# Kernel tuning notes

Measured on AMD Instinct MI355X. Metric: run time of the kernel, lower is better.

Reference implementation:

```python
import jax, jax.numpy as jnp
import numpy as np

S, D_IN, D_OUT = 4096, 1024, 1024

def setup_inputs() -> dict:
    key = jax.random.key(0)
    kx, kq, kk, kv = jax.random.split(key, 4)
    scale = 0.02
    return {
        "x": jax.random.normal(kx, (S, D_IN), dtype=jnp.float32),
        "W_query": jax.random.normal(kq, (D_IN, D_OUT), dtype=jnp.float32) * scale,
        "W_key": jax.random.normal(kk, (D_IN, D_OUT), dtype=jnp.float32) * scale,
        "W_value": jax.random.normal(kv, (D_IN, D_OUT), dtype=jnp.float32) * scale,
    }

def reference(x, W_query, W_key, W_value):
    # x: [S, d_in]; W_*: [d_in, d_out]
    queries = x @ W_query        # [S, d_out]
    keys = x @ W_key             # [S, d_out]
    values = x @ W_value         # [S, d_out]
    d_k = keys.shape[-1]
    attn_scores = queries @ keys.T            # [S, S]
    attn_weights = jax.nn.softmax(attn_scores / jnp.sqrt(jnp.float32(d_k)), axis=-1)
    context_vec = attn_weights @ values       # [S, d_out]
    return context_vec
```

## Files before the change

kernel.cpp:

```cpp
#include <hip/hip_runtime.h>
#include <hip/hip_bf16.h>

typedef _Float16 f16x8 __attribute__((ext_vector_type(8)));
typedef float f32x4 __attribute__((ext_vector_type(4)));
typedef unsigned short u16;
typedef u16 u16x8 __attribute__((ext_vector_type(8)));
typedef u16 u16x4 __attribute__((ext_vector_type(4)));

__device__ __forceinline__ u16 f2h_bits(float f) {
    _Float16 h = (_Float16)f;
    return __builtin_bit_cast(u16, h);
}
__device__ __forceinline__ float h2f(u16 b) {
    return (float)__builtin_bit_cast(_Float16, b);
}

template <int MODE>
__global__ __launch_bounds__(256, 4) void gemm_bt(
    const u16* __restrict__ A, int lda,
    const u16* __restrict__ B, int ldb,
    u16* __restrict__ C, int ldc,
    int Ksplit, float alpha, size_t c_z_stride,
    int bnW, int bmW, int numPanelX,
    float* __restrict__ rowsum, u16* __restrict__ vt)
{
    __shared__ __attribute__((aligned(16))) u16 As[128 * 32];
    __shared__ __attribute__((aligned(16))) u16 Bs[128 * 32];

    const int t    = threadIdx.x;
    const int lane = t & 63;
    const int wave = t >> 6;
    const int wm   = wave & 1;
    const int wn   = wave >> 1;
    const int l16  = lane & 15;
    const int quad = lane >> 4;

    const int lin = blockIdx.y * gridDim.x + blockIdx.x;
    const int xcd = lin & 7;
    const int idx = lin >> 3;
    const int px  = xcd % numPanelX;
    const int py  = xcd / numPanelX;
    const int bn  = px * bnW + idx % bnW;
    const int bm  = py * bmW + idx / bnW;

    const int kz = blockIdx.z;
    A += (size_t)kz * Ksplit;
    B += (size_t)kz * Ksplit;
    C += (size_t)kz * c_z_stride;

    const int srow = t >> 2;
    const int scol = ((t & 3) ^ ((t >> 3) & 3)) * 8;

    const u16* Ag = A + (size_t)(bm * 128 + srow) * lda + scol;
    const u16* Bg = B + (size_t)(bn * 128 + srow) * ldb + scol;
    const size_t a64 = (size_t)64 * lda;
    const size_t b64 = (size_t)64 * ldb;

    u16* AsD = &As[t * 8];
    u16* BsD = &Bs[t * 8];

    const int fseg = (quad ^ ((l16 >> 1) & 3)) * 8;
    const u16* Afr = &As[(wm * 64 + l16) * 32 + fseg];
    const u16* Bfr = &Bs[(wn * 64 + l16) * 32 + fseg];

    f32x4 acc[4][4] = {};

    float4 a0A, a1A, b0A, b1A;
    float4 a0B, a1B, b0B, b1B;

    a0A = *(const float4*)(Ag);
    a1A = *(const float4*)(Ag + a64);
    b0A = *(const float4*)(Bg);
    b1A = *(const float4*)(Bg + b64);
    a0B = *(const float4*)(Ag + 32);
    a1B = *(const float4*)(Ag + 32 + a64);
    b0B = *(const float4*)(Bg + 32);
    b1B = *(const float4*)(Bg + 32 + b64);

    for (int k0 = 0; k0 < Ksplit; k0 += 64) {
        __syncthreads();
        *(float4*)(AsD)        = a0A;
        *(float4*)(AsD + 2048) = a1A;
        *(float4*)(BsD)        = b0A;
        *(float4*)(BsD + 2048) = b1A;
        __syncthreads();

        {
            const int kn = (k0 + 64 < Ksplit) ? k0 + 64 : 0;
            a0A = *(const float4*)(Ag + kn);
            a1A = *(const float4*)(Ag + kn + a64);
            b0A = *(const float4*)(Bg + kn);
            b1A = *(const float4*)(Bg + kn + b64);
        }

        {
            f16x8 af[4], bfv[4];
#pragma unroll
            for (int i = 0; i < 4; i++) af[i]  = *(const f16x8*)(Afr + i * 512);
#pragma unroll
            for (int i = 0; i < 4; i++) bfv[i] = *(const f16x8*)(Bfr + i * 512);
#pragma unroll
            for (int mi = 0; mi < 4; mi++)
#pragma unroll
                for (int ni = 0; ni < 4; ni++)
                    acc[mi][ni] = __builtin_amdgcn_mfma_f32_16x16x32_f16(
                        af[mi], bfv[ni], acc[mi][ni], 0, 0, 0);
        }

        __syncthreads();
        *(float4*)(AsD)        = a0B;
        *(float4*)(AsD + 2048) = a1B;
        *(float4*)(BsD)        = b0B;
        *(float4*)(BsD + 2048) = b1B;
        __syncthreads();

        {
            const int kn = (k0 + 96 < Ksplit) ? k0 + 96 : 0;
            a0B = *(const float4*)(Ag + kn);
            a1B = *(const float4*)(Ag + kn + a64);
            b0B = *(const float4*)(Bg + kn);
            b1B = *(const float4*)(Bg + kn + b64);
        }

        {
            f16x8 af[4], bfv[4];
#pragma unroll
            for (int i = 0; i < 4; i++) af[i]  = *(const f16x8*)(Afr + i * 512);
#pragma unroll
            for (int i = 0; i < 4; i++) bfv[i] = *(const f16x8*)(Bfr + i * 512);
#pragma unroll
            for (int mi = 0; mi < 4; mi++)
#pragma unroll
                for (int ni = 0; ni < 4; ni++)
                    acc[mi][ni] = __builtin_amdgcn_mfma_f32_16x16x32_f16(
                        af[mi], bfv[ni], acc[mi][ni], 0, 0, 0);
        }
    }

    const int crow = bm * 128 + wm * 64 + quad * 4;
    const int ccol = bn * 128 + wn * 64 + l16;

    if (MODE == 1) {
        float rs[4][4];
#pragma unroll
        for (int mi = 0; mi < 4; mi++)
#pragma unroll
            for (int r = 0; r < 4; r++) rs[mi][r] = 0.f;
#pragma unroll
        for (int mi = 0; mi < 4; mi++) {
#pragma unroll
            for (int ni = 0; ni < 4; ni++) {
#pragma unroll
                for (int r = 0; r < 4; r++) {
                    float e = __expf(acc[mi][ni][r] * alpha);
                    rs[mi][r] += e;
                    C[(size_t)(crow + mi * 16 + r) * ldc + (ccol + ni * 16)] = f2h_bits(e);
                }
            }
        }
#pragma unroll
        for (int mi = 0; mi < 4; mi++) {
#pragma unroll
            for (int r = 0; r < 4; r++) {
                float s = rs[mi][r];
#pragma unroll
                for (int o = 1; o < 16; o <<= 1) s += __shfl_xor(s, o);
                if (l16 == 0)
                    atomicAdd(&rowsum[crow + mi * 16 + r], s);
            }
        }
    } else if (MODE == 2 && bn >= 16) {
#pragma unroll
        for (int ni = 0; ni < 4; ni++) {
            const int cV = (bn - 16) * 128 + wn * 64 + ni * 16 + l16;
#pragma unroll
            for (int mi = 0; mi < 4; mi++) {
                u16x4 o;
#pragma unroll
                for (int r = 0; r < 4; r++) o[r] = f2h_bits(acc[mi][ni][r]);
                *(u16x4*)(vt + (size_t)cV * 4096 + crow + mi * 16) = o;
            }
        }
    } else {
#pragma unroll
        for (int mi = 0; mi < 4; mi++)
#pragma unroll
            for (int ni = 0; ni < 4; ni++)
#pragma unroll
                for (int r = 0; r < 4; r++)
                    C[(size_t)(crow + mi * 16 + r) * ldc + (ccol + ni * 16)] =
                        f2h_bits(acc[mi][ni][r] * alpha);
    }
}

__global__ __launch_bounds__(256) void cast_to_f16(
    const float* __restrict__ in, u16* __restrict__ out, int n)
{
    int i = (blockIdx.x * 256 + threadIdx.x) * 4;
    if (i + 3 < n) {
        float4 v = *(const float4*)(in + i);
        ushort4 o;
        o.x = f2h_bits(v.x);
        o.y = f2h_bits(v.y);
        o.z = f2h_bits(v.z);
        o.w = f2h_bits(v.w);
        *(ushort4*)(out + i) = o;
    }
}

__global__ __launch_bounds__(256) void transpose_w3(
    const float* __restrict__ W0, const float* __restrict__ W1,
    const float* __restrict__ W2, u16* __restrict__ out)
{
    const float* in = (blockIdx.z == 0) ? W0 : (blockIdx.z == 1) ? W1 : W2;
    u16* o = out + (size_t)blockIdx.z * 1024 * 1024;
    __shared__ float tile[32][33];
    const int bx = blockIdx.x * 32;
    const int by = blockIdx.y * 32;
    const int tx = threadIdx.x, ty = threadIdx.y;
#pragma unroll
    for (int j = 0; j < 4; j++)
        tile[ty + j * 8][tx] = in[(size_t)(by + ty + j * 8) * 1024 + bx + tx];
    __syncthreads();
#pragma unroll
    for (int j = 0; j < 4; j++)
        o[(size_t)(bx + ty + j * 8) * 1024 + by + tx] = f2h_bits(tile[tx][ty + j * 8]);
}

__global__ __launch_bounds__(256) void zero_f32(float* __restrict__ p, int n)
{
    int i = (blockIdx.x * 256 + threadIdx.x) * 4;
    if (i + 3 < n) *(float4*)(p + i) = float4{0.f, 0.f, 0.f, 0.f};
}

__global__ __launch_bounds__(256) void add_div4(
    const u16* __restrict__ P, const float* __restrict__ l,
    float* __restrict__ o)
{
    const size_t zs = (size_t)4096 * 1024;
    int i = (blockIdx.x * 256 + threadIdx.x) * 8;
    float inv = 1.0f / l[i >> 10];
    float s[8] = {};
#pragma unroll
    for (int z = 0; z < 4; z++) {
        u16x8 h = *(const u16x8*)(P + z * zs + i);
#pragma unroll
        for (int j = 0; j < 8; j++) s[j] += h2f(h[j]);
    }
    float4 lo{s[0] * inv, s[1] * inv, s[2] * inv, s[3] * inv};
    float4 hi{s[4] * inv, s[5] * inv, s[6] * inv, s[7] * inv};
    *(float4*)(o + i) = lo;
    *(float4*)(o + i + 4) = hi;
}

extern "C" void kernel_launch(void* const* d_in, const int* in_sizes, int n_in,
                              void* d_out, int out_size, void* d_ws, size_t ws_size,
                              hipStream_t stream)
{
    (void)in_sizes; (void)n_in; (void)out_size; (void)ws_size;
    const float* x  = (const float*)d_in[0];
    const float* Wq = (const float*)d_in[1];
    const float* Wk = (const float*)d_in[2];
    const float* Wv = (const float*)d_in[3];
    float* out = (float*)d_out;
    char* ws = (char*)d_ws;

    u16* xb  = (u16*)(ws);
    u16* Wt  = (u16*)(ws + ((size_t)8  << 20));
    u16* QK  = (u16*)(ws + ((size_t)14 << 20));
    u16* Sb  = (u16*)(ws + ((size_t)32 << 20));
    u16* Vt  = (u16*)(ws + ((size_t)64 << 20));
    float* lr = (float*)(ws + ((size_t)72 << 20));
    u16* P   = (u16*)(ws);

    const int S = 4096, D = 1024;
    dim3 tb(32, 8);

    cast_to_f16<<<(S * D) / (4 * 256), 256, 0, stream>>>(x, xb, S * D);

    transpose_w3<<<dim3(32, 32, 3), tb, 0, stream>>>(Wq, Wk, Wv, Wt);

    gemm_bt<2><<<dim3(3072 / 128, S / 128, 1), 256, 0, stream>>>(
        xb, D, Wt, D, QK, 2048, D, 1.0f, 0, 6, 16, 4, nullptr, Vt);

    zero_f32<<<S / (4 * 256), 256, 0, stream>>>(lr, S);

    gemm_bt<1><<<dim3(S / 128, S / 128, 1), 256, 0, stream>>>(
        QK, 2048, QK + 1024, 2048, Sb, S, D, 0.03125f, 0, 8, 16, 4, lr, nullptr);

    gemm_bt<0><<<dim3(D / 128, S / 128, 4), 256, 0, stream>>>(
        Sb, S, Vt, S, P, D, 1024, 1.0f, (size_t)S * D, 4, 8, 2, nullptr, nullptr);

    add_div4<<<(S * D) / (8 * 256), 256, 0, stream>>>(P, lr, out);
}
```

Before: 223.9 us.

## Rewrite GEMM as 256x256 tiles with direct global-to-LDS async double buffering

Replaces the 128x128, 4-wave GEMM with a 256x256, 8-wave tile that loads global memory straight into LDS via global_load_lds, double-buffered two k-tiles ahead with explicit vmcnt waits. The MFMA loop is split into four quadrant phases separated by barriers and setprio so LDS fragment reads and prefetches interleave with matrix ops. The aim is to cut register staging, raise arithmetic intensity per tile and hide memory latency. In exchange it uses 128KB of LDS per block, holds a larger accumulator, and launches fewer blocks (e.g. 192 for the QKV GEMM), which may underfill the GPU.

```diff
diff --git a/kernel.cpp b/kernel.cpp
--- a/kernel.cpp
+++ b/kernel.cpp
@@ -1,5 +1,4 @@
 #include <hip/hip_runtime.h>
-#include <hip/hip_bf16.h>
 
 typedef _Float16 f16x8 __attribute__((ext_vector_type(8)));
 typedef float f32x4 __attribute__((ext_vector_type(4)));
@@ -15,8 +14,14 @@
     return (float)__builtin_bit_cast(_Float16, b);
 }
 
+typedef __attribute__((address_space(1))) unsigned int gu32_as1;
+typedef __attribute__((address_space(3))) unsigned int lu32_as3;
+__device__ __forceinline__ void gload16(const u16* g, u16* l) {
+    __builtin_amdgcn_global_load_lds((gu32_as1*)g, (lu32_as3*)l, 16, 0, 0);
+}
+
 template <int MODE>
-__global__ __launch_bounds__(256, 4) void gemm_bt(
+__global__ __launch_bounds__(512, 2) void gemm_bt(
     const u16* __restrict__ A, int lda,
     const u16* __restrict__ B, int ldb,
     u16* __restrict__ C, int ldc,
@@ -24,14 +29,14 @@
     int bnW, int bmW, int numPanelX,
     float* __restrict__ rowsum, u16* __restrict__ vt)
 {
-    __shared__ __attribute__((aligned(16))) u16 As[128 * 32];
-    __shared__ __attribute__((aligned(16))) u16 Bs[128 * 32];
+    __shared__ __attribute__((aligned(16))) u16 As[32768];
+    __shared__ __attribute__((aligned(16))) u16 Bs[32768];
 
     const int t    = threadIdx.x;
     const int lane = t & 63;
     const int wave = t >> 6;
-    const int wm   = wave & 1;
-    const int wn   = wave >> 1;
+    const int wm   = wave >> 2;
+    const int wn   = wave & 3;
     const int l16  = lane & 15;
     const int quad = lane >> 4;
 
@@ -49,105 +54,151 @@
     C += (size_t)kz * c_z_stride;
 
     const int srow = t >> 2;
-    const int scol = ((t & 3) ^ ((t >> 3) & 3)) * 8;
-
-    const u16* Ag = A + (size_t)(bm * 128 + srow) * lda + scol;
-    const u16* Bg = B + (size_t)(bn * 128 + srow) * ldb + scol;
-    const size_t a64 = (size_t)64 * lda;
-    const size_t b64 = (size_t)64 * ldb;
-
-    u16* AsD = &As[t * 8];
-    u16* BsD = &Bs[t * 8];
-
-    const int fseg = (quad ^ ((l16 >> 1) & 3)) * 8;
-    const u16* Afr = &As[(wm * 64 + l16) * 32 + fseg];
-    const u16* Bfr = &Bs[(wn * 64 + l16) * 32 + fseg];
-
-    f32x4 acc[4][4] = {};
-
-    float4 a0A, a1A, b0A, b1A;
-    float4 a0B, a1B, b0B, b1B;
-
-    a0A = *(const float4*)(Ag);
-    a1A = *(const float4*)(Ag + a64);
-    b0A = *(const float4*)(Bg);
-    b1A = *(const float4*)(Bg + b64);
-    a0B = *(const float4*)(Ag + 32);
-    a1B = *(const float4*)(Ag + 32 + a64);
-    b0B = *(const float4*)(Bg + 32);
-    b1B = *(const float4*)(Bg + 32 + b64);
-
-    for (int k0 = 0; k0 < Ksplit; k0 += 64) {
-        __syncthreads();
-        *(float4*)(AsD)        = a0A;
-        *(float4*)(AsD + 2048) = a1A;
-        *(float4*)(BsD)        = b0A;
-        *(float4*)(BsD + 2048) = b1A;
-        __syncthreads();
-
-        {
-            const int kn = (k0 + 64 < Ksplit) ? k0 + 64 : 0;
-            a0A = *(const float4*)(Ag + kn);
-            a1A = *(const float4*)(Ag + kn + a64);
-            b0A = *(const float4*)(Bg + kn);
-            b1A = *(const float4*)(Bg + kn + b64);
-        }
-
-        {
-            f16x8 af[4], bfv[4];
-#pragma unroll
-            for (int i = 0; i < 4; i++) af[i]  = *(const f16x8*)(Afr + i * 512);
-#pragma unroll
-            for (int i = 0; i < 4; i++) bfv[i] = *(const f16x8*)(Bfr + i * 512);
-#pragma unroll
-            for (int mi = 0; mi < 4; mi++)
-#pragma unroll
-                for (int ni = 0; ni < 4; ni++)
-                    acc[mi][ni] = __builtin_amdgcn_mfma_f32_16x16x32_f16(
-                        af[mi], bfv[ni], acc[mi][ni], 0, 0, 0);
-        }
-
-        __syncthreads();
-        *(float4*)(AsD)        = a0B;
-        *(float4*)(AsD + 2048) = a1B;
-        *(float4*)(BsD)        = b0B;
-        *(float4*)(BsD + 2048) = b1B;
-        __syncthreads();
-
-        {
-            const int kn = (k0 + 96 < Ksplit) ? k0 + 96 : 0;
-            a0B = *(const float4*)(Ag + kn);
-            a1B = *(const float4*)(Ag + kn + a64);
-            b0B = *(const float4*)(Bg + kn);
-            b1B = *(const float4*)(Bg + kn + b64);
-        }
-
-        {
-            f16x8 af[4], bfv[4];
-#pragma unroll
-            for (int i = 0; i < 4; i++) af[i]  = *(const f16x8*)(Afr + i * 512);
-#pragma unroll
-            for (int i = 0; i < 4; i++) bfv[i] = *(const f16x8*)(Bfr + i * 512);
-#pragma unroll
-            for (int mi = 0; mi < 4; mi++)
-#pragma unroll
-                for (int ni = 0; ni < 4; ni++)
-                    acc[mi][ni] = __builtin_amdgcn_mfma_f32_16x16x32_f16(
-                        af[mi], bfv[ni], acc[mi][ni], 0, 0, 0);
-        }
+    const int sseg = (t & 3) ^ ((t >> 3) & 3);
+
+    const u16* gA = A + (size_t)(bm * 256 + srow) * lda + sseg * 8;
+    const u16* gB = B + (size_t)(bn * 256 + srow) * ldb + sseg * 8;
+    const size_t a128 = (size_t)128 * lda;
+    const size_t b128 = (size_t)128 * ldb;
+
+    u16* lA = As + t * 8;
+    u16* lB = Bs + t * 8;
+
+#define STAGE_A(bufv, kt) do {                                   \
+        const u16* _g = gA + (size_t)(kt) * 64;                  \
+        u16* _l = lA + (bufv) * 16384;                           \
+        gload16(_g,             _l);                             \
+        gload16(_g + 32,        _l + 4096);                      \
+        gload16(_g + a128,      _l + 8192);                      \
+        gload16(_g + a128 + 32, _l + 12288);                     \
+    } while (0)
+#define STAGE_B(bufv, kt) do {                                   \
+        const u16* _g = gB + (size_t)(kt) * 64;                  \
+        u16* _l = lB + (bufv) * 16384;                           \
+        gload16(_g,             _l);                             \
+        gload16(_g + 32,        _l + 4096);                      \
+        gload16(_g + b128,      _l + 8192);                      \
+        gload16(_g + b128 + 32, _l + 12288);                     \
+    } while (0)
+
+    const int fslot = quad ^ ((l16 >> 1) & 3);
+    const u16* Afr = As + wm * 8192 + l16 * 32 + fslot * 8;
+    const u16* Bfr = Bs + (wn >> 1) * 8192 + (wn & 1) * 2048 + l16 * 32 + fslot * 8;
+
+    f32x4 acc[8][4] = {};
+
+    const int NT = Ksplit >> 6;
+
+    STAGE_A(0, 0); STAGE_B(0, 0);
+    STAGE_A(1, 1); STAGE_B(1, 1);
+    asm volatile("s_waitcnt vmcnt(8)" ::: "memory");
+    __builtin_amdgcn_sched_barrier(0);
+    __builtin_amdgcn_s_barrier();
+
+    int buf = 0;
+    for (int kt = 0; kt < NT; ++kt, buf ^= 1) {
+        const u16* Af = Afr + buf * 16384;
+        const u16* Bf = Bfr + buf * 16384;
+        f16x8 af[4][2], bfA[2][2], bfB[2][2];
+
+#pragma unroll
+        for (int mi = 0; mi < 4; mi++)
+#pragma unroll
+            for (int kk = 0; kk < 2; kk++)
+                af[mi][kk] = *(const f16x8*)(Af + kk * 4096 + mi * 512);
+#pragma unroll
+        for (int nj = 0; nj < 2; nj++)
+#pragma unroll
+            for (int kk = 0; kk < 2; kk++)
+                bfA[nj][kk] = *(const f16x8*)(Bf + kk * 4096 + nj * 512);
+        __builtin_amdgcn_sched_barrier(0);
+        __builtin_amdgcn_s_barrier();
+        __builtin_amdgcn_s_setprio(1);
+#pragma unroll
+        for (int mi = 0; mi < 4; mi++)
+#pragma unroll
+            for (int nj = 0; nj < 2; nj++)
+#pragma unroll
+                for (int kk = 0; kk < 2; kk++)
+                    acc[mi][nj] = __builtin_amdgcn_mfma_f32_16x16x32_f16(
+                        af[mi][kk], bfA[nj][kk], acc[mi][nj], 0, 0, 0);
+        __builtin_amdgcn_s_setprio(0);
+        __builtin_amdgcn_sched_barrier(0);
+        __builtin_amdgcn_s_barrier();
+
+#pragma unroll
+        for (int nj = 0; nj < 2; nj++)
+#pragma unroll
+            for (int kk = 0; kk < 2; kk++)
+                bfB[nj][kk] = *(const f16x8*)(Bf + kk * 4096 + (2 + nj) * 512);
+        __builtin_amdgcn_sched_barrier(0);
+        __builtin_amdgcn_s_barrier();
+        __builtin_amdgcn_s_setprio(1);
+#pragma unroll
+        for (int mi = 0; mi < 4; mi++)
+#pragma unroll
+            for (int nj = 0; nj < 2; nj++)
+#pragma unroll
+                for (int kk = 0; kk < 2; kk++)
+                    acc[mi][2 + nj] = __builtin_amdgcn_mfma_f32_16x16x32_f16(
+                        af[mi][kk], bfB[nj][kk], acc[mi][2 + nj], 0, 0, 0);
+        __builtin_amdgcn_s_setprio(0);
+        __builtin_amdgcn_sched_barrier(0);
+        __builtin_amdgcn_s_barrier();
+
+#pragma unroll
+        for (int mi = 0; mi < 4; mi++)
+#pragma unroll
+            for (int kk = 0; kk < 2; kk++)
+                af[mi][kk] = *(const f16x8*)(Af + kk * 4096 + (4 + mi) * 512);
+        if (kt + 2 < NT) STAGE_B(buf, kt + 2);
+        __builtin_amdgcn_sched_barrier(0);
+        __builtin_amdgcn_s_barrier();
+        __builtin_amdgcn_s_setprio(1);
+#pragma unroll
+        for (int mi = 0; mi < 4; mi++)
+#pragma unroll
+            for (int nj = 0; nj < 2; nj++)
+#pragma unroll
+                for (int kk = 0; kk < 2; kk++)
+                    acc[4 + mi][nj] = __builtin_amdgcn_mfma_f32_16x16x32_f16(
+                        af[mi][kk], bfA[nj][kk], acc[4 + mi][nj], 0, 0, 0);
+        __builtin_amdgcn_s_setprio(0);
+        __builtin_amdgcn_sched_barrier(0);
+        __builtin_amdgcn_s_barrier();
+
+        if (kt + 2 < NT) STAGE_A(buf, kt + 2);
+        __builtin_amdgcn_sched_barrier(0);
+        __builtin_amdgcn_s_barrier();
+        __builtin_amdgcn_s_setprio(1);
+#pragma unroll
+        for (int mi = 0; mi < 4; mi++)
+#pragma unroll
+            for (int nj = 0; nj < 2; nj++)
+#pragma unroll
+                for (int kk = 0; kk < 2; kk++)
+                    acc[4 + mi][2 + nj] = __builtin_amdgcn_mfma_f32_16x16x32_f16(
+                        af[mi][kk], bfB[nj][kk], acc[4 + mi][2 + nj], 0, 0, 0);
+        __builtin_amdgcn_s_setprio(0);
+        if (kt < NT - 2)       asm volatile("s_waitcnt vmcnt(8)" ::: "memory");
+        else if (kt == NT - 2) asm volatile("s_waitcnt vmcnt(0)" ::: "memory");
+        __builtin_amdgcn_sched_barrier(0);
+        __builtin_amdgcn_s_barrier();
     }
-
-    const int crow = bm * 128 + wm * 64 + quad * 4;
-    const int ccol = bn * 128 + wn * 64 + l16;
+#undef STAGE_A
+#undef STAGE_B
+
+    const int crow = bm * 256 + wm * 128 + quad * 4;
+    const int ccol = bn * 256 + wn * 64 + l16;
 
     if (MODE == 1) {
-        float rs[4][4];
-#pragma unroll
-        for (int mi = 0; mi < 4; mi++)
+        float rs[8][4];
+#pragma unroll
+        for (int mi = 0; mi < 8; mi++)
 #pragma unroll
             for (int r = 0; r < 4; r++) rs[mi][r] = 0.f;
 #pragma unroll
-        for (int mi = 0; mi < 4; mi++) {
+        for (int mi = 0; mi < 8; mi++) {
 #pragma unroll
             for (int ni = 0; ni < 4; ni++) {
 #pragma unroll
@@ -159,7 +210,7 @@
             }
         }
 #pragma unroll
-        for (int mi = 0; mi < 4; mi++) {
+        for (int mi = 0; mi < 8; mi++) {
 #pragma unroll
             for (int r = 0; r < 4; r++) {
                 float s = rs[mi][r];
@@ -169,12 +220,12 @@
                     atomicAdd(&rowsum[crow + mi * 16 + r], s);
             }
         }
-    } else if (MODE == 2 && bn >= 16) {
+    } else if (MODE == 2 && bn >= 8) {
 #pragma unroll
         for (int ni = 0; ni < 4; ni++) {
-            const int cV = (bn - 16) * 128 + wn * 64 + ni * 16 + l16;
-#pragma unroll
-            for (int mi = 0; mi < 4; mi++) {
+            const int cV = (bn - 8) * 256 + wn * 64 + ni * 16 + l16;
+#pragma unroll
+            for (int mi = 0; mi < 8; mi++) {
                 u16x4 o;
 #pragma unroll
                 for (int r = 0; r < 4; r++) o[r] = f2h_bits(acc[mi][ni][r]);
@@ -183,7 +234,7 @@
         }
     } else {
 #pragma unroll
-        for (int mi = 0; mi < 4; mi++)
+        for (int mi = 0; mi < 8; mi++)
 #pragma unroll
             for (int ni = 0; ni < 4; ni++)
 #pragma unroll
@@ -280,16 +331,16 @@
 
     transpose_w3<<<dim3(32, 32, 3), tb, 0, stream>>>(Wq, Wk, Wv, Wt);
 
-    gemm_bt<2><<<dim3(3072 / 128, S / 128, 1), 256, 0, stream>>>(
-        xb, D, Wt, D, QK, 2048, D, 1.0f, 0, 6, 16, 4, nullptr, Vt);
+    gemm_bt<2><<<dim3(12, 16, 1), 512, 0, stream>>>(
+        xb, D, Wt, D, QK, 2048, D, 1.0f, 0, 3, 8, 4, nullptr, Vt);
 
     zero_f32<<<S / (4 * 256), 256, 0, stream>>>(lr, S);
 
-    gemm_bt<1><<<dim3(S / 128, S / 128, 1), 256, 0, stream>>>(
-        QK, 2048, QK + 1024, 2048, Sb, S, D, 0.03125f, 0, 8, 16, 4, lr, nullptr);
-
-    gemm_bt<0><<<dim3(D / 128, S / 128, 4), 256, 0, stream>>>(
-        Sb, S, Vt, S, P, D, 1024, 1.0f, (size_t)S * D, 4, 8, 2, nullptr, nullptr);
+    gemm_bt<1><<<dim3(16, 16, 1), 512, 0, stream>>>(
+        QK, 2048, QK + 1024, 2048, Sb, S, D, 0.03125f, 0, 4, 8, 4, lr, nullptr);
+
+    gemm_bt<0><<<dim3(4, 16, 4), 512, 0, stream>>>(
+        Sb, S, Vt, S, P, D, 1024, 1.0f, (size_t)S * D, 1, 8, 4, nullptr, nullptr);
 
     add_div4<<<(S * D) / (8 * 256), 256, 0, stream>>>(P, lr, out);
 }
```

New measurement: 219.6 us. Within noise of the previous version (-1.9%).

## Stage GEMM tiles with direct global-to-LDS loads into a double buffer

Applied to the files above, without the earlier changes.

Tile staging in the GEMM main loop changes from register prefetch followed by LDS stores to the global_load_lds builtin, which writes 16 bytes per lane straight into shared memory. Shared memory is split into two buffers, so the next K-tile loads into one while MFMAs read the other, with one barrier per 32-wide K step instead of two. This frees the staging VGPRs and the LDS store instructions. In exchange it doubles LDS use per block, and it depends on the compiler inserting the right vmcnt waits before the barrier so that async LDS writes are complete before the data is read.

```diff
diff --git a/kernel.cpp b/kernel.cpp
--- a/kernel.cpp
+++ b/kernel.cpp
@@ -1,5 +1,4 @@
 #include <hip/hip_runtime.h>
-#include <hip/hip_bf16.h>
 
 typedef _Float16 f16x8 __attribute__((ext_vector_type(8)));
 typedef float f32x4 __attribute__((ext_vector_type(4)));
@@ -13,6 +12,12 @@
 }
 __device__ __forceinline__ float h2f(u16 b) {
     return (float)__builtin_bit_cast(_Float16, b);
+}
+
+typedef __attribute__((address_space(1))) unsigned int gu32_as1;
+typedef __attribute__((address_space(3))) unsigned int lu32_as3;
+__device__ __forceinline__ void gload16(const u16* g, u16* l) {
+    __builtin_amdgcn_global_load_lds((gu32_as1*)g, (lu32_as3*)l, 16, 0, 0);
 }
 
 template <int MODE>
@@ -24,8 +29,8 @@
     int bnW, int bmW, int numPanelX,
     float* __restrict__ rowsum, u16* __restrict__ vt)
 {
-    __shared__ __attribute__((aligned(16))) u16 As[128 * 32];
-    __shared__ __attribute__((aligned(16))) u16 Bs[128 * 32];
+    __shared__ __attribute__((aligned(16))) u16 As[8192];
+    __shared__ __attribute__((aligned(16))) u16 Bs[8192];
 
     const int t    = threadIdx.x;
     const int lane = t & 63;
@@ -59,83 +64,43 @@
     u16* AsD = &As[t * 8];
     u16* BsD = &Bs[t * 8];
 
+#define STAGE(bufv, k0) do {                                     \
+        gload16(Ag + (k0),       AsD + (bufv) * 4096);           \
+        gload16(Ag + (k0) + a64, AsD + (bufv) * 4096 + 2048);    \
+        gload16(Bg + (k0),       BsD + (bufv) * 4096);           \
+        gload16(Bg + (k0) + b64, BsD + (bufv) * 4096 + 2048);    \
+    } while (0)
+
     const int fseg = (quad ^ ((l16 >> 1) & 3)) * 8;
     const u16* Afr = &As[(wm * 64 + l16) * 32 + fseg];
     const u16* Bfr = &Bs[(wn * 64 + l16) * 32 + fseg];
 
     f32x4 acc[4][4] = {};
 
-    float4 a0A, a1A, b0A, b1A;
-    float4 a0B, a1B, b0B, b1B;
-
-    a0A = *(const float4*)(Ag);
-    a1A = *(const float4*)(Ag + a64);
-    b0A = *(const float4*)(Bg);
-    b1A = *(const float4*)(Bg + b64);
-    a0B = *(const float4*)(Ag + 32);
-    a1B = *(const float4*)(Ag + 32 + a64);
-    b0B = *(const float4*)(Bg + 32);
-    b1B = *(const float4*)(Bg + 32 + b64);
-
-    for (int k0 = 0; k0 < Ksplit; k0 += 64) {
+    const int NT = Ksplit >> 5;
+
+    STAGE(0, 0);
+
+    for (int k = 0; k < NT; ++k) {
+        const int cur = k & 1;
         __syncthreads();
-        *(float4*)(AsD)        = a0A;
-        *(float4*)(AsD + 2048) = a1A;
-        *(float4*)(BsD)        = b0A;
-        *(float4*)(BsD + 2048) = b1A;
-        __syncthreads();
-
-        {
-            const int kn = (k0 + 64 < Ksplit) ? k0 + 64 : 0;
-            a0A = *(const float4*)(Ag + kn);
-            a1A = *(const float4*)(Ag + kn + a64);
-            b0A = *(const float4*)(Bg + kn);
-            b1A = *(const float4*)(Bg + kn + b64);
-        }
-
-        {
-            f16x8 af[4], bfv[4];
-#pragma unroll
-            for (int i = 0; i < 4; i++) af[i]  = *(const f16x8*)(Afr + i * 512);
-#pragma unroll
-            for (int i = 0; i < 4; i++) bfv[i] = *(const f16x8*)(Bfr + i * 512);
-#pragma unroll
-            for (int mi = 0; mi < 4; mi++)
-#pragma unroll
-                for (int ni = 0; ni < 4; ni++)
-                    acc[mi][ni] = __builtin_amdgcn_mfma_f32_16x16x32_f16(
-                        af[mi], bfv[ni], acc[mi][ni], 0, 0, 0);
-        }
-
-        __syncthreads();
-        *(float4*)(AsD)        = a0B;
-        *(float4*)(AsD + 2048) = a1B;
-        *(float4*)(BsD)        = b0B;
-        *(float4*)(BsD + 2048) = b1B;
-        __syncthreads();
-
-        {
-            const int kn = (k0 + 96 < Ksplit) ? k0 + 96 : 0;
-            a0B = *(const float4*)(Ag + kn);
-            a1B = *(const float4*)(Ag + kn + a64);
-            b0B = *(const float4*)(Bg + kn);
-            b1B = *(const float4*)(Bg + kn + b64);
-        }
-
-        {
-            f16x8 af[4], bfv[4];
-#pragma unroll
-            for (int i = 0; i < 4; i++) af[i]  = *(const f16x8*)(Afr + i * 512);
-#pragma unroll
-            for (int i = 0; i < 4; i++) bfv[i] = *(const f16x8*)(Bfr + i * 512);
-#pragma unroll
-            for (int mi = 0; mi < 4; mi++)
-#pragma unroll
-                for (int ni = 0; ni < 4; ni++)
-                    acc[mi][ni] = __builtin_amdgcn_mfma_f32_16x16x32_f16(
-                        af[mi], bfv[ni], acc[mi][ni], 0, 0, 0);
-        }
-    }
+        if (k + 1 < NT) STAGE(cur ^ 1, (k + 1) * 32);
+
+        f16x8 af[4], bfv[4];
+#pragma unroll
+        for (int i = 0; i < 4; i++)
+            af[i]  = *(const f16x8*)(Afr + cur * 4096 + i * 512);
+#pragma unroll
+        for (int i = 0; i < 4; i++)
+            bfv[i] = *(const f16x8*)(Bfr + cur * 4096 + i * 512);
+#pragma unroll
+        for (int mi = 0; mi < 4; mi++)
+#pragma unroll
+            for (int ni = 0; ni < 4; ni++)
+                acc[mi][ni] = __builtin_amdgcn_mfma_f32_16x16x32_f16(
+                    af[mi], bfv[ni], acc[mi][ni], 0, 0, 0);
+    }
+#undef STAGE
 
     const int crow = bm * 128 + wm * 64 + quad * 4;
     const int ccol = bn * 128 + wn * 64 + l16;
```

New measurement: 224.2 us. Within noise of the previous version (+0.1%).
